# Performance work log

Measured on AMD Instinct MI355X. Metric: run time of the kernel, lower is better.

## Reference

```python
import jax, jax.numpy as jnp
import numpy as np

B, T, I, H, L, C = 64, 512, 128, 512, 3, 5


def setup_inputs() -> dict:
    key = jax.random.key(0)
    ks = jax.random.split(key, 2 + 4 * L + 2)
    s = 1.0 / np.sqrt(H)  # PyTorch RNN init range
    inp = {"x": jax.random.normal(ks[0], (B, T, I), dtype=jnp.float32)}
    in_dims = [I] + [H] * (L - 1)
    for l in range(L):
        k0, k1, k2, k3 = ks[1 + 4 * l:5 + 4 * l]
        inp[f"W_ih{l}"] = jax.random.uniform(k0, (H, in_dims[l]), jnp.float32, -s, s)
        inp[f"W_hh{l}"] = jax.random.uniform(k1, (H, H), jnp.float32, -s, s)
        inp[f"b_ih{l}"] = jax.random.uniform(k2, (H,), jnp.float32, -s, s)
        inp[f"b_hh{l}"] = jax.random.uniform(k3, (H,), jnp.float32, -s, s)
    so = 1.0 / np.sqrt(H)
    inp["W_out"] = jax.random.uniform(ks[-2], (C, H), jnp.float32, -so, so)
    inp["b_out"] = jax.random.uniform(ks[-1], (C,), jnp.float32, -so, so)
    return inp


def _rnn_layer(xs, W_ih, W_hh, b_ih, b_hh):
    # xs: [B, T, D] -> hidden sequence [B, T, H], ReLU RNN recurrence
    h0 = jnp.zeros((xs.shape[0], W_hh.shape[0]), xs.dtype)
    xproj = jnp.einsum('btd,hd->bth', xs, W_ih) + (b_ih + b_hh)  # precompute input GEMM

    def step(h, xp_t):
        h = jax.nn.relu(xp_t + h @ W_hh.T)
        return h, h

    _, ys = jax.lax.scan(step, h0, jnp.swapaxes(xproj, 0, 1))  # scan over time
    return jnp.swapaxes(ys, 0, 1)


def reference(x, W_ih0, W_hh0, b_ih0, b_hh0, W_ih1, W_hh1, b_ih1, b_hh1,
              W_ih2, W_hh2, b_ih2, b_hh2, W_out, b_out):
    h = x
    for W_ih, W_hh, b_ih, b_hh in ((W_ih0, W_hh0, b_ih0, b_hh0),
                                   (W_ih1, W_hh1, b_ih1, b_hh1),
                                   (W_ih2, W_hh2, b_ih2, b_hh2)):
        h = _rnn_layer(h, W_ih, W_hh, b_ih, b_hh)
    # last timestep -> linear head: [B, C]
    return h[:, -1, :] @ W_out.T + b_out
```

## Files before the change

### kernel.cpp

```cpp
#include <hip/hip_runtime.h>

#define BB 64
#define TT 512
#define II 128
#define HH 512
#define CC 5

__global__ __launch_bounds__(256) void gemm_bias_kernel(
    const float* __restrict__ A, const float* __restrict__ W,
    const float* __restrict__ b1, const float* __restrict__ b2,
    float* __restrict__ out, int K)
{
    __shared__ float As[16][132];
    __shared__ float Bs[16][132];
    const int tid = threadIdx.x;
    const int bm = blockIdx.x;
    const int bn = blockIdx.y;
    const int tx = tid & 15;
    const int ty = tid >> 4;
    const int lr = tid >> 2;
    const int lk = (tid & 3) << 2;

    const float* Ab = A + (size_t)bm * 128 * K;
    const float* Wb = W + (size_t)bn * 128 * K;

    float acc[8][8];
#pragma unroll
    for (int i = 0; i < 8; ++i)
#pragma unroll
        for (int j = 0; j < 8; ++j) acc[i][j] = 0.f;

    for (int k0 = 0; k0 < K; k0 += 16) {
        float4 a0 = *(const float4*)(Ab + (size_t)lr * K + k0 + lk);
        float4 a1 = *(const float4*)(Ab + (size_t)(lr + 64) * K + k0 + lk);
        float4 w0 = *(const float4*)(Wb + (size_t)lr * K + k0 + lk);
        float4 w1 = *(const float4*)(Wb + (size_t)(lr + 64) * K + k0 + lk);
        __syncthreads();
        As[lk + 0][lr] = a0.x; As[lk + 1][lr] = a0.y; As[lk + 2][lr] = a0.z; As[lk + 3][lr] = a0.w;
        As[lk + 0][lr + 64] = a1.x; As[lk + 1][lr + 64] = a1.y; As[lk + 2][lr + 64] = a1.z; As[lk + 3][lr + 64] = a1.w;
        Bs[lk + 0][lr] = w0.x; Bs[lk + 1][lr] = w0.y; Bs[lk + 2][lr] = w0.z; Bs[lk + 3][lr] = w0.w;
        Bs[lk + 0][lr + 64] = w1.x; Bs[lk + 1][lr + 64] = w1.y; Bs[lk + 2][lr + 64] = w1.z; Bs[lk + 3][lr + 64] = w1.w;
        __syncthreads();
#pragma unroll
        for (int k = 0; k < 16; ++k) {
            float4 av0 = *(const float4*)&As[k][ty * 8];
            float4 av1 = *(const float4*)&As[k][ty * 8 + 4];
            float4 bv0 = *(const float4*)&Bs[k][tx * 8];
            float4 bv1 = *(const float4*)&Bs[k][tx * 8 + 4];
            float a[8] = {av0.x, av0.y, av0.z, av0.w, av1.x, av1.y, av1.z, av1.w};
            float b[8] = {bv0.x, bv0.y, bv0.z, bv0.w, bv1.x, bv1.y, bv1.z, bv1.w};
#pragma unroll
            for (int i = 0; i < 8; ++i)
#pragma unroll
                for (int j = 0; j < 8; ++j)
                    acc[i][j] = fmaf(a[i], b[j], acc[i][j]);
        }
    }

    const int nb = bn * 128 + tx * 8;
    float bias[8];
#pragma unroll
    for (int j = 0; j < 8; ++j) bias[j] = b1[nb + j] + b2[nb + j];
#pragma unroll
    for (int i = 0; i < 8; ++i) {
        const size_t m = (size_t)bm * 128 + ty * 8 + i;
        float4 o0 = {acc[i][0] + bias[0], acc[i][1] + bias[1], acc[i][2] + bias[2], acc[i][3] + bias[3]};
        float4 o1 = {acc[i][4] + bias[4], acc[i][5] + bias[5], acc[i][6] + bias[6], acc[i][7] + bias[7]};
        *(float4*)(out + m * HH + nb) = o0;
        *(float4*)(out + m * HH + nb + 4) = o1;
    }
}

__global__ __launch_bounds__(512)
__attribute__((amdgpu_waves_per_eu(2, 2)))
void scan_kernel(
    const float* __restrict__ xp, const float* __restrict__ Whh,
    float* __restrict__ y, unsigned long long* hbuf)
{
    __shared__ float hbs[2][2][8 * 68];

    const int tid  = threadIdx.x;
    const int s    = blockIdx.x >> 5;
    const int g    = blockIdx.x & 31;
    const int lane = tid & 63;
    const int wv   = tid >> 6;
    const int rloc = lane >> 3;
    const int kseg = lane & 7;
    const int R    = s * 64 + wv * 8 + rloc;

    const float* wr = Whh + (size_t)R * HH + kseg * 64;
    const float4 w0  = *(const float4*)(wr + 0);
    const float4 w1  = *(const float4*)(wr + 4);
    const float4 w2  = *(const float4*)(wr + 8);
    const float4 w3  = *(const float4*)(wr + 12);
    const float4 w4  = *(const float4*)(wr + 16);
    const float4 w5  = *(const float4*)(wr + 20);
    const float4 w6  = *(const float4*)(wr + 24);
    const float4 w7  = *(const float4*)(wr + 28);
    const float4 w8  = *(const float4*)(wr + 32);
    const float4 w9  = *(const float4*)(wr + 36);
    const float4 w10 = *(const float4*)(wr + 40);
    const float4 w11 = *(const float4*)(wr + 44);
    const float4 w12 = *(const float4*)(wr + 48);
    const float4 w13 = *(const float4*)(wr + 52);
    const float4 w14 = *(const float4*)(wr + 56);
    const float4 w15 = *(const float4*)(wr + 60);

    unsigned long long* gbase = hbuf + (size_t)g * 1024;
    const int gb0 = g * 2, gb1 = g * 2 + 1;

    const int lds_w    = wv * 68 + lane;
    const int self_lds = s * 68 + wv * 8 + rloc;
    const bool pub     = (kseg == 0);
    const bool foreign = (wv != s);

    hbs[0][0][lds_w] = 0.f;
    hbs[0][1][lds_w] = 0.f;

    float xp0 = 0.f, xp1 = 0.f;
    if (pub) {
        xp0 = xp[(size_t)gb0 * TT * HH + R];
        xp1 = xp[(size_t)gb1 * TT * HH + R];
    }
    __syncthreads();

    for (int t = 0; t < TT; ++t) {
        const int p = t & 1;

        float a0 = 0.f, a1 = 0.f, c0 = 0.f, c1 = 0.f;
        const float* h0p = &hbs[p][0][kseg * 68];
        const float* h1p = &hbs[p][1][kseg * 68];
#define STEP4(WQ, OFF)                                                   \
        {                                                                \
            float4 h0 = *(const float4*)(h0p + (OFF));                   \
            float4 h1 = *(const float4*)(h1p + (OFF));                   \
            a0 = fmaf(WQ.x, h0.x, a0); a1 = fmaf(WQ.y, h0.y, a1);        \
            a0 = fmaf(WQ.z, h0.z, a0); a1 = fmaf(WQ.w, h0.w, a1);        \
            c0 = fmaf(WQ.x, h1.x, c0); c1 = fmaf(WQ.y, h1.y, c1);        \
            c0 = fmaf(WQ.z, h1.z, c0); c1 = fmaf(WQ.w, h1.w, c1);        \
        }
        STEP4(w0, 0)   STEP4(w1, 4)   STEP4(w2, 8)   STEP4(w3, 12)
        STEP4(w4, 16)  STEP4(w5, 20)  STEP4(w6, 24)  STEP4(w7, 28)
        STEP4(w8, 32)  STEP4(w9, 36)  STEP4(w10, 40) STEP4(w11, 44)
        STEP4(w12, 48) STEP4(w13, 52) STEP4(w14, 56) STEP4(w15, 60)
#undef STEP4

        float A = a0 + a1, Bv = c0 + c1;
        A  += __shfl_xor(A, 1);  A  += __shfl_xor(A, 2);  A  += __shfl_xor(A, 4);
        Bv += __shfl_xor(Bv, 1); Bv += __shfl_xor(Bv, 2); Bv += __shfl_xor(Bv, 4);

        const int q = t + 1;
        unsigned long long* slotp = gbase + (q & 1) * 512;
        const unsigned int phase = (unsigned int)(((q + 1) >> 1) & 1);

        if (pub) {
            const float hn0 = fmaxf(A + xp0, 0.f);
            const float hn1 = fmaxf(Bv + xp1, 0.f);
            if (q < TT) {
                const unsigned long long pkt =
                    (unsigned long long)(__float_as_uint(hn0) | (phase << 31)) |
                    ((unsigned long long)(__float_as_uint(hn1) | (phase << 31)) << 32);
                __hip_atomic_store(slotp + R, pkt,
                                   __ATOMIC_RELAXED, __HIP_MEMORY_SCOPE_AGENT);
            }
            hbs[q & 1][0][self_lds] = hn0;
            hbs[q & 1][1][self_lds] = hn1;
            y[((size_t)gb0 * TT + t) * HH + R] = hn0;
            y[((size_t)gb1 * TT + t) * HH + R] = hn1;
            if (q < TT) {
                xp0 = xp[((size_t)gb0 * TT + q) * HH + R];
                xp1 = xp[((size_t)gb1 * TT + q) * HH + R];
            }
        }

        if (foreign && q < TT) {
            unsigned long long u;
            for (;;) {
                u = __hip_atomic_load(slotp + tid, __ATOMIC_RELAXED, __HIP_MEMORY_SCOPE_AGENT);
                if ((((unsigned int)(u >> 31) & 1u) == phase) &&
                    ((unsigned int)(u >> 63) == phase)) break;
            }
            hbs[q & 1][0][lds_w] = __uint_as_float((unsigned int)u & 0x7fffffffu);
            hbs[q & 1][1][lds_w] = __uint_as_float((unsigned int)(u >> 32) & 0x7fffffffu);
        }
        __syncthreads();
    }
}

__global__ __launch_bounds__(64) void head_kernel(
    const float* __restrict__ y2, const float* __restrict__ Wout,
    const float* __restrict__ bout, float* __restrict__ out)
{
    const int bc = blockIdx.x;
    const int b = bc / CC, c = bc % CC;
    const int lane = threadIdx.x;
    const float* yrow = y2 + ((size_t)b * TT + (TT - 1)) * HH;
    const float* wrow = Wout + (size_t)c * HH;
    float s = 0.f;
#pragma unroll
    for (int i = 0; i < HH / 64; ++i)
        s = fmaf(yrow[lane + 64 * i], wrow[lane + 64 * i], s);
#pragma unroll
    for (int off = 32; off > 0; off >>= 1) s += __shfl_down(s, off);
    if (lane == 0) out[bc] = s + bout[c];
}

extern "C" void kernel_launch(void* const* d_in, const int* in_sizes, int n_in,
                              void* d_out, int out_size, void* d_ws, size_t ws_size,
                              hipStream_t stream)
{
    const float* x = (const float*)d_in[0];
    const float* W_ih[3] = {(const float*)d_in[1], (const float*)d_in[5], (const float*)d_in[9]};
    const float* W_hh[3] = {(const float*)d_in[2], (const float*)d_in[6], (const float*)d_in[10]};
    const float* b_ih[3] = {(const float*)d_in[3], (const float*)d_in[7], (const float*)d_in[11]};
    const float* b_hh[3] = {(const float*)d_in[4], (const float*)d_in[8], (const float*)d_in[12]};
    const float* W_out = (const float*)d_in[13];
    const float* b_out = (const float*)d_in[14];
    float* out = (float*)d_out;

    float* ws   = (float*)d_ws;
    float* Y    = ws;
    float* XP   = ws + (size_t)BB * TT * HH;
    unsigned long long* hbuf = (unsigned long long*)(XP + (size_t)BB * TT * HH);

    const size_t hbuf_bytes = 32 * 2 * 512 * sizeof(unsigned long long);
    const dim3 ggrid(256, 4, 1);

    gemm_bias_kernel<<<ggrid, 256, 0, stream>>>(x, W_ih[0], b_ih[0], b_hh[0], XP, II);
    hipMemsetAsync(hbuf, 0, hbuf_bytes, stream);
    scan_kernel<<<256, 512, 0, stream>>>(XP, W_hh[0], Y, hbuf);
    gemm_bias_kernel<<<ggrid, 256, 0, stream>>>(Y, W_ih[1], b_ih[1], b_hh[1], XP, HH);
    hipMemsetAsync(hbuf, 0, hbuf_bytes, stream);
    scan_kernel<<<256, 512, 0, stream>>>(XP, W_hh[1], Y, hbuf);
    gemm_bias_kernel<<<ggrid, 256, 0, stream>>>(Y, W_ih[2], b_ih[2], b_hh[2], XP, HH);
    hipMemsetAsync(hbuf, 0, hbuf_bytes, stream);
    scan_kernel<<<256, 512, 0, stream>>>(XP, W_hh[2], Y, hbuf);
    head_kernel<<<BB * CC, 64, 0, stream>>>(Y, W_out, b_out, out);
}
```

Measured before the change: 3.194 ms.

## Replace per-step block barrier with LDS progress counters and 4-deep buffers

The per-timestep __syncthreads in the recurrent scan is replaced by per-wave progress counters in shared memory. Each wave spins until every wave has published step t before it reads the hidden state. The LDS and global hidden-state rings grow from 2 to 4 slots, with a phase scheme adjusted to match, so waves can drift apart without overwriting data still being read. This targets barrier stalls on the serial critical path, at the cost of spin polling on LDS and subtler memory-ordering correctness.

```diff
diff --git a/kernel.cpp b/kernel.cpp
--- a/kernel.cpp
+++ b/kernel.cpp
@@ -77,7 +77,8 @@
     const float* __restrict__ xp, const float* __restrict__ Whh,
     float* __restrict__ y, unsigned long long* hbuf)
 {
-    __shared__ float hbs[2][2][8 * 68];
+    __shared__ float hbs[4][2][8 * 68];
+    __shared__ int written[8];
 
     const int tid  = threadIdx.x;
     const int s    = blockIdx.x >> 5;
@@ -106,7 +107,7 @@
     const float4 w14 = *(const float4*)(wr + 56);
     const float4 w15 = *(const float4*)(wr + 60);
 
-    unsigned long long* gbase = hbuf + (size_t)g * 1024;
+    unsigned long long* gbase = hbuf + (size_t)g * 2048;
     const int gb0 = g * 2, gb1 = g * 2 + 1;
 
     const int lds_w    = wv * 68 + lane;
@@ -116,6 +117,7 @@
 
     hbs[0][0][lds_w] = 0.f;
     hbs[0][1][lds_w] = 0.f;
+    if (tid < 8) written[tid] = 0;
 
     float xp0 = 0.f, xp1 = 0.f;
     if (pub) {
@@ -125,11 +127,25 @@
     __syncthreads();
 
     for (int t = 0; t < TT; ++t) {
-        const int p = t & 1;
-
+        if (t > 0) {
+            for (;;) {
+                int m = __hip_atomic_load(&written[0], __ATOMIC_RELAXED,
+                                          __HIP_MEMORY_SCOPE_WORKGROUP);
+#pragma unroll
+                for (int c = 1; c < 8; ++c) {
+                    int wc = __hip_atomic_load(&written[c], __ATOMIC_RELAXED,
+                                               __HIP_MEMORY_SCOPE_WORKGROUP);
+                    m = (wc < m) ? wc : m;
+                }
+                if (m >= t) break;
+            }
+            __threadfence_block();
+        }
+
+        const int bi = t & 3;
         float a0 = 0.f, a1 = 0.f, c0 = 0.f, c1 = 0.f;
-        const float* h0p = &hbs[p][0][kseg * 68];
-        const float* h1p = &hbs[p][1][kseg * 68];
+        const float* h0p = &hbs[bi][0][kseg * 68];
+        const float* h1p = &hbs[bi][1][kseg * 68];
 #define STEP4(WQ, OFF)                                                   \
         {                                                                \
             float4 h0 = *(const float4*)(h0p + (OFF));                   \
@@ -150,21 +166,22 @@
         Bv += __shfl_xor(Bv, 1); Bv += __shfl_xor(Bv, 2); Bv += __shfl_xor(Bv, 4);
 
         const int q = t + 1;
-        unsigned long long* slotp = gbase + (q & 1) * 512;
-        const unsigned int phase = (unsigned int)(((q + 1) >> 1) & 1);
-
+        unsigned long long* slotp = gbase + (q & 3) * 512;
+        const unsigned int phase = 1u ^ (((unsigned)(q - 1) >> 2) & 1u);
+
+        float hn0 = 0.f, hn1 = 0.f;
         if (pub) {
-            const float hn0 = fmaxf(A + xp0, 0.f);
-            const float hn1 = fmaxf(Bv + xp1, 0.f);
+            hn0 = fmaxf(A + xp0, 0.f);
+            hn1 = fmaxf(Bv + xp1, 0.f);
             if (q < TT) {
                 const unsigned long long pkt =
                     (unsigned long long)(__float_as_uint(hn0) | (phase << 31)) |
                     ((unsigned long long)(__float_as_uint(hn1) | (phase << 31)) << 32);
                 __hip_atomic_store(slotp + R, pkt,
                                    __ATOMIC_RELAXED, __HIP_MEMORY_SCOPE_AGENT);
-            }
-            hbs[q & 1][0][self_lds] = hn0;
-            hbs[q & 1][1][self_lds] = hn1;
+                hbs[q & 3][0][self_lds] = hn0;
+                hbs[q & 3][1][self_lds] = hn1;
+            }
             y[((size_t)gb0 * TT + t) * HH + R] = hn0;
             y[((size_t)gb1 * TT + t) * HH + R] = hn1;
             if (q < TT) {
@@ -173,17 +190,23 @@
             }
         }
 
-        if (foreign && q < TT) {
-            unsigned long long u;
-            for (;;) {
-                u = __hip_atomic_load(slotp + tid, __ATOMIC_RELAXED, __HIP_MEMORY_SCOPE_AGENT);
-                if ((((unsigned int)(u >> 31) & 1u) == phase) &&
-                    ((unsigned int)(u >> 63) == phase)) break;
-            }
-            hbs[q & 1][0][lds_w] = __uint_as_float((unsigned int)u & 0x7fffffffu);
-            hbs[q & 1][1][lds_w] = __uint_as_float((unsigned int)(u >> 32) & 0x7fffffffu);
-        }
-        __syncthreads();
+        if (q < TT) {
+            if (foreign) {
+                unsigned long long u;
+                for (;;) {
+                    u = __hip_atomic_load(slotp + tid, __ATOMIC_RELAXED,
+                                          __HIP_MEMORY_SCOPE_AGENT);
+                    if ((((unsigned int)(u >> 31) & 1u) == phase) &&
+                        ((unsigned int)(u >> 63) == phase)) break;
+                }
+                hbs[q & 3][0][lds_w] = __uint_as_float((unsigned int)u & 0x7fffffffu);
+                hbs[q & 3][1][lds_w] = __uint_as_float((unsigned int)(u >> 32) & 0x7fffffffu);
+            }
+            __threadfence_block();
+            if (lane == 0)
+                __hip_atomic_store(&written[wv], q, __ATOMIC_RELAXED,
+                                   __HIP_MEMORY_SCOPE_WORKGROUP);
+        }
     }
 }
 
@@ -223,17 +246,17 @@
     float* XP   = ws + (size_t)BB * TT * HH;
     unsigned long long* hbuf = (unsigned long long*)(XP + (size_t)BB * TT * HH);
 
-    const size_t hbuf_bytes = 32 * 2 * 512 * sizeof(unsigned long long);
+    const size_t hbuf_bytes = 32 * 4 * 512 * sizeof(unsigned long long);
     const dim3 ggrid(256, 4, 1);
 
     gemm_bias_kernel<<<ggrid, 256, 0, stream>>>(x, W_ih[0], b_ih[0], b_hh[0], XP, II);
-    hipMemsetAsync(hbuf, 0, hbuf_bytes, stream);
+    (void)hipMemsetAsync(hbuf, 0, hbuf_bytes, stream);
     scan_kernel<<<256, 512, 0, stream>>>(XP, W_hh[0], Y, hbuf);
     gemm_bias_kernel<<<ggrid, 256, 0, stream>>>(Y, W_ih[1], b_ih[1], b_hh[1], XP, HH);
-    hipMemsetAsync(hbuf, 0, hbuf_bytes, stream);
+    (void)hipMemsetAsync(hbuf, 0, hbuf_bytes, stream);
     scan_kernel<<<256, 512, 0, stream>>>(XP, W_hh[1], Y, hbuf);
     gemm_bias_kernel<<<ggrid, 256, 0, stream>>>(Y, W_ih[2], b_ih[2], b_hh[2], XP, HH);
-    hipMemsetAsync(hbuf, 0, hbuf_bytes, stream);
+    (void)hipMemsetAsync(hbuf, 0, hbuf_bytes, stream);
     scan_kernel<<<256, 512, 0, stream>>>(XP, W_hh[2], Y, hbuf);
     head_kernel<<<BB * CC, 64, 0, stream>>>(Y, W_out, b_out, out);
 }
```

Result: faster. 2.688 ms (-15.8%).
